# Kernel optimization log

Hardware: AMD Instinct MI355X
Metric: run time of the kernel (lower is better)

Reference implementation:

```python
import jax, jax.numpy as jnp
import numpy as np

SLOPE = 25.0   # fast_sigmoid surrogate slope
BETA = 0.9     # LIF decay
THR = 1.0      # snntorch default threshold
STEPS = 10


@jax.custom_vjp
def spike(x):
    # Heaviside forward, fast-sigmoid surrogate backward
    return (x > 0).astype(x.dtype)

def _spike_fwd(x):
    return spike(x), x

def _spike_bwd(x, g):
    return (g / (SLOPE * jnp.abs(x) + 1.0) ** 2,)

spike.defvjp(_spike_fwd, _spike_bwd)


def lif(inp, mem):
    # snntorch Leaky, reset_mechanism='subtract': reset based on previous mem, detached
    reset = jax.lax.stop_gradient((mem > THR).astype(mem.dtype))
    mem = BETA * mem + inp - reset * THR
    spk = spike(mem - THR)
    return spk, mem


def setup_inputs() -> dict:
    key = jax.random.key(0)
    ks = jax.random.split(key, 4)
    B, IN, H, O = 65536, 512, 1024, 1
    x = jax.random.normal(ks[0], (B, IN), dtype=jnp.float32)
    W1 = jax.random.normal(ks[1], (IN, H), dtype=jnp.float32) / np.sqrt(IN)
    b1 = jnp.zeros((H,), jnp.float32)
    W2 = jax.random.normal(ks[2], (H, H), dtype=jnp.float32) / np.sqrt(H)
    b2 = jnp.zeros((H,), jnp.float32)
    Wo = jax.random.normal(ks[3], (H, O), dtype=jnp.float32) / np.sqrt(H)
    bo = jnp.zeros((O,), jnp.float32)
    return {"x": x, "W1": W1, "b1": b1, "W2": W2, "b2": b2, "Wo": Wo, "bo": bo}


def reference(x, W1, b1, W2, b2, Wo, bo):
    # fc1(x) is identical every timestep (x is static input current)
    cur1 = x @ W1 + b1                      # [B, H]
    B = x.shape[0]
    H = W1.shape[1]
    O = Wo.shape[1]
    m1 = jnp.zeros((B, H), x.dtype)
    m2 = jnp.zeros((B, H), x.dtype)
    mo = jnp.zeros((B, O), x.dtype)

    def step(carry, _):
        m1, m2, mo = carry
        s1, m1 = lif(cur1, m1)
        s2, m2 = lif(s1 @ W2 + b2, m2)
        _, mo = lif(s2 @ Wo + bo, mo)
        return (m1, m2, mo), mo

    _, recs = jax.lax.scan(step, (m1, m2, mo), None, length=STEPS)  # [STEPS, B, O]
    return recs.mean(0)
```

## Files before the change

### kernel.cpp

```cpp
#include <hip/hip_runtime.h>
#include <cstdint>
#include <cstddef>


typedef _Float16 f16;
typedef _Float16 f16x8 __attribute__((ext_vector_type(8)));
typedef float f32x4 __attribute__((ext_vector_type(4)));
typedef int i32x4 __attribute__((ext_vector_type(4)));

#define MFMA16(A, B, C) __builtin_amdgcn_mfma_f32_16x16x32_f16(A, B, C, 0, 0, 0)

static constexpr int BSZ = 65536;
static constexpr int IN = 512;
static constexpr int H = 1024;

__global__ void prep_dekker(const float* __restrict__ src, f16* __restrict__ dst) {
    int idx = blockIdx.x * 256 + threadIdx.x;
    int k = idx >> 10;
    int j = idx & 1023;
    float w = src[(size_t)k * 1024 + j];
    f16 hi = (f16)w;
    float lo = (w - (float)hi) * 2048.0f;
    size_t o = (size_t)j * 1024 + k;
    dst[o] = hi;
    dst[o + (size_t)H * H] = (f16)lo;
}

__global__ __launch_bounds__(256, 2) void k1_chain(
    const float* __restrict__ x, const float* __restrict__ w1,
    const float* __restrict__ b1, unsigned short* __restrict__ s1b) {
    __shared__ float xs[32][65];
    __shared__ float ws[32][256];
    const int hblk = blockIdx.x;
    const int bblk = blockIdx.y;
    const int tid = threadIdx.x;
    const int ht = tid & 15, bt = tid >> 4;
    const int h0 = hblk * 256, b0 = bblk * 64;

    float acc[4][16] = {};

    for (int kc = 0; kc < 512; kc += 32) {
        float4 xv[2], wv[8];
#pragma unroll
        for (int i = 0; i < 2; ++i) {
            int idx = tid + 256 * i;
            int br = idx >> 3, ks = idx & 7;
            xv[i] = *(const float4*)&x[(size_t)(b0 + br) * IN + kc + ks * 4];
        }
#pragma unroll
        for (int i = 0; i < 8; ++i) {
            int idx = tid + 256 * i;
            int kr = idx >> 6, c4 = idx & 63;
            wv[i] = *(const float4*)&w1[(size_t)(kc + kr) * H + h0 + c4 * 4];
        }
        __syncthreads();
#pragma unroll
        for (int i = 0; i < 2; ++i) {
            int idx = tid + 256 * i;
            int br = idx >> 3, ks = idx & 7;
            xs[ks * 4 + 0][br] = xv[i].x;
            xs[ks * 4 + 1][br] = xv[i].y;
            xs[ks * 4 + 2][br] = xv[i].z;
            xs[ks * 4 + 3][br] = xv[i].w;
        }
#pragma unroll
        for (int i = 0; i < 8; ++i) {
            int idx = tid + 256 * i;
            int kr = idx >> 6, c4 = idx & 63;
            *(float4*)&ws[kr][c4 * 4] = wv[i];
        }
        __syncthreads();
#pragma unroll
        for (int k = 0; k < 32; ++k) {
            float xr[4];
#pragma unroll
            for (int i = 0; i < 4; ++i) xr[i] = xs[k][bt * 4 + i];
            float wr[16];
#pragma unroll
            for (int g = 0; g < 4; ++g) {
                float4 t = *(const float4*)&ws[k][ht * 16 + g * 4];
                wr[g * 4 + 0] = t.x; wr[g * 4 + 1] = t.y;
                wr[g * 4 + 2] = t.z; wr[g * 4 + 3] = t.w;
            }
#pragma unroll
            for (int i = 0; i < 4; ++i)
#pragma unroll
                for (int j = 0; j < 16; ++j)
                    acc[i][j] = fmaf(xr[i], wr[j], acc[i][j]);
        }
    }

    float b1v[16];
#pragma unroll
    for (int j = 0; j < 16; ++j) b1v[j] = b1[h0 + ht * 16 + j];
#pragma unroll
    for (int i = 0; i < 4; ++i) {
        unsigned short outb[16];
#pragma unroll
        for (int j = 0; j < 16; ++j) {
            float c = __fadd_rn(acc[i][j], b1v[j]);
            float m = 0.0f;
            unsigned bits = 0u;
#pragma unroll
            for (int t = 0; t < 10; ++t) {
                float rst = (m > 1.0f) ? 1.0f : 0.0f;
                m = __fmul_rn(0.9f, m);
                m = __fadd_rn(m, c);
                m = __fsub_rn(m, rst);
                if (m > 1.0f) bits |= (1u << t);
            }
            outb[j] = (unsigned short)bits;
        }
        size_t off = (size_t)(b0 + bt * 4 + i) * H + h0 + ht * 16;
        *(int4*)&s1b[off] = ((const int4*)outb)[0];
        *(int4*)&s1b[off + 8] = ((const int4*)outb)[1];
    }
}

__global__ __launch_bounds__(512, 4) void k2_spikes_gemm(
    const unsigned short* __restrict__ s1bits, const f16* __restrict__ w2d,
    const float* __restrict__ b2, const float* __restrict__ wo,
    float* __restrict__ po) {
    __shared__ i32x4 AL[2][2][4][64];
    __shared__ i32x4 BL[2][2][2][2][64];
    __shared__ float m2x[4][64][8];
    const int jblk = blockIdx.x, bblk = blockIdx.y;
    const int tid = threadIdx.x;
    const int lane = tid & 63, wave = tid >> 6;
    const int strip = wave & 3, thalf = wave >> 2;
    const int l15 = lane & 15, loct = lane >> 4;
    const int t0 = thalf * 5;

    const bool stageB = (tid >= 256);
    const int s = tid & 255;
    const int sl15 = s & 15, sseg = (s >> 4) & 3;
    const int slot = (sseg << 4) | sl15;
    const int astrip = s >> 6;
    const int bp = (s >> 7) & 1, bcf = (s >> 6) & 1;

    const char* gsrc;
    if (stageB)
        gsrc = (const char*)(w2d + (size_t)bp * H * H
                             + (size_t)(jblk * 32 + bcf * 16 + sl15) * 1024 + sseg * 8);
    else
        gsrc = (const char*)(s1bits + (size_t)(bblk * 64 + astrip * 16 + sl15) * 1024 + sseg * 8);

    f32x4 acc[5][2][2] = {};

    i32x4 gv0 = *(const i32x4*)(gsrc);
    i32x4 gv1 = *(const i32x4*)(gsrc + 64);

    typedef union { i32x4 i; unsigned long long u[2]; f16x8 h; } U;

    int buf = 0;
    for (int kc = 0; kc < 1024; kc += 64) {
        if (stageB) {
            BL[buf][0][bp][bcf][slot] = gv0;
            BL[buf][1][bp][bcf][slot] = gv1;
        } else {
            AL[buf][0][astrip][slot] = gv0;
            AL[buf][1][astrip][slot] = gv1;
        }
        int kn = (kc + 64) & 1023;
        i32x4 gn0 = *(const i32x4*)(gsrc + kn * 2);
        i32x4 gn1 = *(const i32x4*)(gsrc + kn * 2 + 64);
        __syncthreads();
#pragma unroll
        for (int kch = 0; kch < 2; ++kch) {
            U m;
            m.i = AL[buf][kch][strip][lane];
            f16x8 bf[2][2];
#pragma unroll
            for (int p = 0; p < 2; ++p)
#pragma unroll
                for (int cf = 0; cf < 2; ++cf) {
                    U b; b.i = BL[buf][kch][p][cf][lane];
                    bf[p][cf] = b.h;
                }
#pragma unroll
            for (int tt = 0; tt < 5; ++tt) {
                const int sh = 10 - (t0 + tt);
                U r;
                r.u[0] = (m.u[0] << sh) & 0x0400040004000400ULL;
                r.u[1] = (m.u[1] << sh) & 0x0400040004000400ULL;
                acc[tt][0][0] = MFMA16(r.h, bf[0][0], acc[tt][0][0]);
                acc[tt][0][1] = MFMA16(r.h, bf[0][1], acc[tt][0][1]);
                acc[tt][1][0] = MFMA16(r.h, bf[1][0], acc[tt][1][0]);
                acc[tt][1][1] = MFMA16(r.h, bf[1][1], acc[tt][1][1]);
            }
        }
        gv0 = gn0; gv1 = gn1;
        buf ^= 1;
    }

    int col0 = jblk * 32 + l15;
    float b2v0 = b2[col0], b2v1 = b2[col0 + 16];
    double wov0 = (double)wo[col0], wov1 = (double)wo[col0 + 16];
    int rowb = bblk * 64 + strip * 16 + loct * 4;
    float m2a[4] = {0.0f, 0.0f, 0.0f, 0.0f};
    float m2b[4] = {0.0f, 0.0f, 0.0f, 0.0f};

    if (thalf == 0) {
#pragma unroll
        for (int tt = 0; tt < 5; ++tt) {
#pragma unroll
            for (int r = 0; r < 4; ++r) {
                float i0 = (float)((double)acc[tt][0][0][r] * 16384.0 + (double)acc[tt][1][0][r] * 8.0);
                i0 = __fadd_rn(i0, b2v0);
                float rst0 = (m2a[r] > 1.0f) ? 1.0f : 0.0f;
                m2a[r] = __fmul_rn(0.9f, m2a[r]);
                m2a[r] = __fadd_rn(m2a[r], i0);
                m2a[r] = __fsub_rn(m2a[r], rst0);
                float i1 = (float)((double)acc[tt][0][1][r] * 16384.0 + (double)acc[tt][1][1][r] * 8.0);
                i1 = __fadd_rn(i1, b2v1);
                float rst1 = (m2b[r] > 1.0f) ? 1.0f : 0.0f;
                m2b[r] = __fmul_rn(0.9f, m2b[r]);
                m2b[r] = __fadd_rn(m2b[r], i1);
                m2b[r] = __fsub_rn(m2b[r], rst1);
                double pv = ((m2a[r] > 1.0f) ? wov0 : 0.0) + ((m2b[r] > 1.0f) ? wov1 : 0.0);
                pv += __shfl_xor(pv, 1);
                pv += __shfl_xor(pv, 2);
                pv += __shfl_xor(pv, 4);
                pv += __shfl_xor(pv, 8);
                if (l15 == r)
                    po[(size_t)(tt * 32 + jblk) * BSZ + rowb + r] = (float)pv;
            }
        }
#pragma unroll
        for (int r = 0; r < 4; ++r) {
            m2x[strip][lane][r] = m2a[r];
            m2x[strip][lane][4 + r] = m2b[r];
        }
    }
    __syncthreads();
    if (thalf == 1) {
#pragma unroll
        for (int r = 0; r < 4; ++r) {
            m2a[r] = m2x[strip][lane][r];
            m2b[r] = m2x[strip][lane][4 + r];
        }
#pragma unroll
        for (int tt = 0; tt < 5; ++tt) {
#pragma unroll
            for (int r = 0; r < 4; ++r) {
                float i0 = (float)((double)acc[tt][0][0][r] * 16384.0 + (double)acc[tt][1][0][r] * 8.0);
                i0 = __fadd_rn(i0, b2v0);
                float rst0 = (m2a[r] > 1.0f) ? 1.0f : 0.0f;
                m2a[r] = __fmul_rn(0.9f, m2a[r]);
                m2a[r] = __fadd_rn(m2a[r], i0);
                m2a[r] = __fsub_rn(m2a[r], rst0);
                float i1 = (float)((double)acc[tt][0][1][r] * 16384.0 + (double)acc[tt][1][1][r] * 8.0);
                i1 = __fadd_rn(i1, b2v1);
                float rst1 = (m2b[r] > 1.0f) ? 1.0f : 0.0f;
                m2b[r] = __fmul_rn(0.9f, m2b[r]);
                m2b[r] = __fadd_rn(m2b[r], i1);
                m2b[r] = __fsub_rn(m2b[r], rst1);
                double pv = ((m2a[r] > 1.0f) ? wov0 : 0.0) + ((m2b[r] > 1.0f) ? wov1 : 0.0);
                pv += __shfl_xor(pv, 1);
                pv += __shfl_xor(pv, 2);
                pv += __shfl_xor(pv, 4);
                pv += __shfl_xor(pv, 8);
                if (l15 == r)
                    po[(size_t)((5 + tt) * 32 + jblk) * BSZ + rowb + r] = (float)pv;
            }
        }
    }
}

__global__ void k3_out(const float* __restrict__ po, const float* __restrict__ bo,
                       float* __restrict__ out) {
    int b = blockIdx.x * 256 + threadIdx.x;
    float mo = 0.0f, s = 0.0f;
    float bov = bo[0];
    for (int t = 0; t < 10; ++t) {
        float inp = 0.0f;
#pragma unroll
        for (int jb = 0; jb < 32; ++jb) inp += po[(size_t)(t * 32 + jb) * BSZ + b];
        inp = __fadd_rn(inp, bov);
        float rst = (mo > 1.0f) ? 1.0f : 0.0f;
        mo = __fmul_rn(0.9f, mo);
        mo = __fadd_rn(mo, inp);
        mo = __fsub_rn(mo, rst);
        s += mo;
    }
    out[b] = s / 10.0f;
}

extern "C" void kernel_launch(void* const* d_in, const int* in_sizes, int n_in,
                              void* d_out, int out_size, void* d_ws, size_t ws_size,
                              hipStream_t stream) {
    (void)in_sizes; (void)n_in; (void)out_size; (void)ws_size;
    const float* x  = (const float*)d_in[0];
    const float* W1 = (const float*)d_in[1];
    const float* b1 = (const float*)d_in[2];
    const float* W2 = (const float*)d_in[3];
    const float* b2 = (const float*)d_in[4];
    const float* Wo = (const float*)d_in[5];
    const float* bo = (const float*)d_in[6];
    float* out = (float*)d_out;

    char* ws = (char*)d_ws;
    f16* w2d = (f16*)ws;
    unsigned short* s1bits = (unsigned short*)(ws + ((size_t)16 << 20));
    float* po = (float*)(ws + ((size_t)160 << 20));

    prep_dekker<<<dim3((H * H) / 256), 256, 0, stream>>>(W2, w2d);
    k1_chain<<<dim3(4, BSZ / 64), 256, 0, stream>>>(x, W1, b1, s1bits);
    k2_spikes_gemm<<<dim3(H / 32, BSZ / 64), 512, 0, stream>>>(s1bits, w2d, b2, Wo, po);
    k3_out<<<dim3(BSZ / 256), 256, 0, stream>>>(po, bo, out);
}
```

Baseline: 3.320 ms.

## Enlarge k1 batch tile, prefetch next K chunk, relax k2 barrier

The fc1 kernel now gives each block 128 batch rows instead of 64, so every thread holds an 8x16 accumulator. Global loads for the next K chunk are issued before the inner FMA loop so memory latency overlaps compute, and the column mapping is interleaved so shared-memory reads are float4 and bank-friendly. In the spike GEMM kernel, __syncthreads is replaced by a LDS-only waitcnt plus s_barrier, so the prefetch global loads stay in flight across the barrier. The larger tile raises register pressure, which could reduce occupancy or cause spills.

```diff
diff --git a/kernel.cpp b/kernel.cpp
--- a/kernel.cpp
+++ b/kernel.cpp
@@ -29,33 +29,34 @@
 __global__ __launch_bounds__(256, 2) void k1_chain(
     const float* __restrict__ x, const float* __restrict__ w1,
     const float* __restrict__ b1, unsigned short* __restrict__ s1b) {
-    __shared__ float xs[32][65];
+    __shared__ float xs[32][132];
     __shared__ float ws[32][256];
     const int hblk = blockIdx.x;
     const int bblk = blockIdx.y;
     const int tid = threadIdx.x;
     const int ht = tid & 15, bt = tid >> 4;
-    const int h0 = hblk * 256, b0 = bblk * 64;
-
-    float acc[4][16] = {};
+    const int h0 = hblk * 256, b0 = bblk * 128;
+
+    float acc[8][16] = {};
+
+    float4 xv[4], wv[8];
+#pragma unroll
+    for (int i = 0; i < 4; ++i) {
+        int idx = tid + 256 * i;
+        int br = idx >> 3, ks = idx & 7;
+        xv[i] = *(const float4*)&x[(size_t)(b0 + br) * IN + ks * 4];
+    }
+#pragma unroll
+    for (int i = 0; i < 8; ++i) {
+        int idx = tid + 256 * i;
+        int kr = idx >> 6, c4 = idx & 63;
+        wv[i] = *(const float4*)&w1[(size_t)kr * H + h0 + c4 * 4];
+    }
 
     for (int kc = 0; kc < 512; kc += 32) {
-        float4 xv[2], wv[8];
-#pragma unroll
-        for (int i = 0; i < 2; ++i) {
-            int idx = tid + 256 * i;
-            int br = idx >> 3, ks = idx & 7;
-            xv[i] = *(const float4*)&x[(size_t)(b0 + br) * IN + kc + ks * 4];
-        }
-#pragma unroll
-        for (int i = 0; i < 8; ++i) {
-            int idx = tid + 256 * i;
-            int kr = idx >> 6, c4 = idx & 63;
-            wv[i] = *(const float4*)&w1[(size_t)(kc + kr) * H + h0 + c4 * 4];
-        }
         __syncthreads();
 #pragma unroll
-        for (int i = 0; i < 2; ++i) {
+        for (int i = 0; i < 4; ++i) {
             int idx = tid + 256 * i;
             int br = idx >> 3, ks = idx & 7;
             xs[ks * 4 + 0][br] = xv[i].x;
@@ -70,20 +71,30 @@
             *(float4*)&ws[kr][c4 * 4] = wv[i];
         }
         __syncthreads();
-#pragma unroll
+        int kn = (kc + 32) & 511;
+#pragma unroll
+        for (int i = 0; i < 4; ++i) {
+            int idx = tid + 256 * i;
+            int br = idx >> 3, ks = idx & 7;
+            xv[i] = *(const float4*)&x[(size_t)(b0 + br) * IN + kn + ks * 4];
+        }
+#pragma unroll
+        for (int i = 0; i < 8; ++i) {
+            int idx = tid + 256 * i;
+            int kr = idx >> 6, c4 = idx & 63;
+            wv[i] = *(const float4*)&w1[(size_t)(kn + kr) * H + h0 + c4 * 4];
+        }
+#pragma unroll 2
         for (int k = 0; k < 32; ++k) {
-            float xr[4];
-#pragma unroll
-            for (int i = 0; i < 4; ++i) xr[i] = xs[k][bt * 4 + i];
+            float xr[8];
+            *(float4*)&xr[0] = *(const float4*)&xs[k][bt * 8];
+            *(float4*)&xr[4] = *(const float4*)&xs[k][bt * 8 + 4];
             float wr[16];
 #pragma unroll
-            for (int g = 0; g < 4; ++g) {
-                float4 t = *(const float4*)&ws[k][ht * 16 + g * 4];
-                wr[g * 4 + 0] = t.x; wr[g * 4 + 1] = t.y;
-                wr[g * 4 + 2] = t.z; wr[g * 4 + 3] = t.w;
-            }
-#pragma unroll
-            for (int i = 0; i < 4; ++i)
+            for (int g = 0; g < 4; ++g)
+                *(float4*)&wr[g * 4] = *(const float4*)&ws[k][ht * 4 + 64 * g];
+#pragma unroll
+            for (int i = 0; i < 8; ++i)
 #pragma unroll
                 for (int j = 0; j < 16; ++j)
                     acc[i][j] = fmaf(xr[i], wr[j], acc[i][j]);
@@ -92,9 +103,12 @@
 
     float b1v[16];
 #pragma unroll
-    for (int j = 0; j < 16; ++j) b1v[j] = b1[h0 + ht * 16 + j];
-#pragma unroll
-    for (int i = 0; i < 4; ++i) {
+    for (int g = 0; g < 4; ++g)
+#pragma unroll
+        for (int m = 0; m < 4; ++m)
+            b1v[g * 4 + m] = b1[h0 + g * 64 + ht * 4 + m];
+#pragma unroll
+    for (int i = 0; i < 8; ++i) {
         unsigned short outb[16];
 #pragma unroll
         for (int j = 0; j < 16; ++j) {
@@ -111,9 +125,10 @@
             }
             outb[j] = (unsigned short)bits;
         }
-        size_t off = (size_t)(b0 + bt * 4 + i) * H + h0 + ht * 16;
-        *(int4*)&s1b[off] = ((const int4*)outb)[0];
-        *(int4*)&s1b[off + 8] = ((const int4*)outb)[1];
+        size_t row = (size_t)(b0 + bt * 8 + i);
+#pragma unroll
+        for (int g = 0; g < 4; ++g)
+            *(int2*)&s1b[row * H + h0 + g * 64 + ht * 4] = ((const int2*)outb)[g];
     }
 }
 
@@ -164,7 +179,8 @@
         int kn = (kc + 64) & 1023;
         i32x4 gn0 = *(const i32x4*)(gsrc + kn * 2);
         i32x4 gn1 = *(const i32x4*)(gsrc + kn * 2 + 64);
-        __syncthreads();
+        asm volatile("s_waitcnt lgkmcnt(0)" ::: "memory");
+        __builtin_amdgcn_s_barrier();
 #pragma unroll
         for (int kch = 0; kch < 2; ++kch) {
             U m;
@@ -305,7 +321,7 @@
     float* po = (float*)(ws + ((size_t)160 << 20));
 
     prep_dekker<<<dim3((H * H) / 256), 256, 0, stream>>>(W2, w2d);
-    k1_chain<<<dim3(4, BSZ / 64), 256, 0, stream>>>(x, W1, b1, s1bits);
+    k1_chain<<<dim3(4, BSZ / 128), 256, 0, stream>>>(x, W1, b1, s1bits);
     k2_spikes_gemm<<<dim3(H / 32, BSZ / 64), 512, 0, stream>>>(s1bits, w2d, b2, Wo, po);
     k3_out<<<dim3(BSZ / 256), 256, 0, stream>>>(po, bo, out);
 }
```

Result: faster. 3.108 ms (-6.4%).
